# Performance work log

Hardware: AMD Instinct MI355X
Metric: run time of the kernel (lower is better)

The kernel has to match this reference:

```python
import jax, jax.numpy as jnp
import numpy as np
import math

B, S, D, H = 2, 2048, 1024, 16
HD = D // H            # head dim = 64
E, K = 8, 2            # routed experts, top-k
HM = 1024              # moe_inter_dim (multiple_of=256 keeps it)
HS = 1024              # shared expert hidden = moe_inter_dim * n_shared_experts
EPS = 1e-6
TEMP = 1.0


def setup_inputs() -> dict:
    key = jax.random.key(0)
    ks = jax.random.split(key, 16)
    s = 0.02
    x = jax.random.normal(ks[0], (B, S, D), jnp.float32)
    # RoPE angles: theta = 10000
    inv_freq = 1.0 / (10000.0 ** (np.arange(0, HD, 2, dtype=np.float32) / HD))  # (HD//2,)
    ang = np.arange(S, dtype=np.float32)[:, None] * inv_freq[None, :]           # (S, HD//2)
    freqs_cos = jnp.asarray(np.cos(ang))
    freqs_sin = jnp.asarray(np.sin(ang))
    return {
        "x": x,
        "freqs_cos": freqs_cos,
        "freqs_sin": freqs_sin,
        "att_norm_w": jnp.ones((D,), jnp.float32),
        "ffn_norm_w": jnp.ones((D,), jnp.float32),
        "wq": jax.random.normal(ks[1], (D, D), jnp.float32) * s,
        "wk": jax.random.normal(ks[2], (D, D), jnp.float32) * s,
        "wv": jax.random.normal(ks[3], (D, D), jnp.float32) * s,
        "wo": jax.random.normal(ks[4], (D, D), jnp.float32) * s,
        "gate_w": jax.random.normal(ks[5], (E, D), jnp.float32) * s,
        "ew1": jax.random.normal(ks[6], (E, D, HM), jnp.float32) * s,
        "ew2": jax.random.normal(ks[7], (E, HM, D), jnp.float32) * s,
        "ew3": jax.random.normal(ks[8], (E, D, HM), jnp.float32) * s,
        "sw1": jax.random.normal(ks[9], (D, HS), jnp.float32) * s,
        "sw2": jax.random.normal(ks[10], (HS, D), jnp.float32) * s,
        "sw3": jax.random.normal(ks[11], (D, HS), jnp.float32) * s,
    }


def _rmsnorm(x, w):
    return x * jax.lax.rsqrt(jnp.mean(x * x, axis=-1, keepdims=True) + EPS) * w


def _rope(t, cos, sin):
    # t: (B,H,S,HD); rotate pairs (even, odd) like complex multiply
    tr = t.reshape(B, H, S, HD // 2, 2)
    t0, t1 = tr[..., 0], tr[..., 1]
    c = cos[None, None, :, :]
    s_ = sin[None, None, :, :]
    o0 = t0 * c - t1 * s_
    o1 = t0 * s_ + t1 * c
    return jnp.stack([o0, o1], axis=-1).reshape(B, H, S, HD)


def reference(x, freqs_cos, freqs_sin, att_norm_w, ffn_norm_w,
              wq, wk, wv, wo, gate_w, ew1, ew2, ew3, sw1, sw2, sw3):
    # ---- attention sub-block ----
    xn = _rmsnorm(x, att_norm_w)
    q = (xn @ wq).reshape(B, S, H, HD).transpose(0, 2, 1, 3)  # (B,H,S,HD)
    k = (xn @ wk).reshape(B, S, H, HD).transpose(0, 2, 1, 3)
    v = (xn @ wv).reshape(B, S, H, HD).transpose(0, 2, 1, 3)
    q = _rope(q, freqs_cos, freqs_sin)
    k = _rope(k, freqs_cos, freqs_sin)
    scores = jnp.einsum('bhqd,bhkd->bhqk', q, k) / math.sqrt(HD)
    attn = jax.nn.softmax(scores, axis=-1)
    out = jnp.einsum('bhqk,bhkd->bhqd', attn, v)
    out = out.transpose(0, 2, 1, 3).reshape(B, S, D) @ wo
    h = x + out

    # ---- MoE sub-block ----
    xf = _rmsnorm(h, ffn_norm_w).reshape(-1, D)  # (N,D), N=B*S
    # shared expert (SwiGLU)
    shared = (jax.nn.silu(xf @ sw1) * (xf @ sw3)) @ sw2
    # gate (eval mode: no noise)
    g_scores = (xf @ gate_w.T) / TEMP
    probs = jax.nn.softmax(g_scores, axis=-1)          # (N,E)
    vals, idx = jax.lax.top_k(probs, K)                 # (N,K)
    vals = vals / (jnp.sum(vals, axis=-1, keepdims=True) + 1e-9)
    # per-token per-expert weight (equivalent to scatter into expert_mask)
    mask = jnp.sum(jax.nn.one_hot(idx, E, dtype=xf.dtype) * vals[..., None], axis=1)  # (N,E)
    # routed experts: dense per-expert SwiGLU, weighted combine (zero weight => no contribution)
    h1 = jax.nn.silu(jnp.einsum('nd,edh->enh', xf, ew1)) * jnp.einsum('nd,edh->enh', xf, ew3)
    eo = jnp.einsum('enh,ehd->end', h1, ew2)            # (E,N,D)
    y = jnp.einsum('end,ne->nd', eo, mask) + shared
    return h + y.reshape(B, S, D)
```

## Files before the change

### kernel.cpp

```cpp
#include <hip/hip_runtime.h>
#include <hip/hip_bf16.h>
#include <stdint.h>


typedef __hip_bfloat16 bf16;
typedef __attribute__((ext_vector_type(8))) __bf16 bf16x8;
typedef __attribute__((ext_vector_type(4))) float f32x4;
typedef __attribute__((ext_vector_type(2))) unsigned int u32x2;

#define S_  2048
#define D_  1024
#define N_  4096

__device__ __forceinline__ float b2f(bf16 h) { return __bfloat162float(h); }
__device__ __forceinline__ bf16  f2b(float f) { return __float2bfloat16(f); }

__device__ __forceinline__ bf16x8 ld_bf16x8(const bf16* p) {
    union { uint4 u; bf16x8 v; } x;
    x.u = *(const uint4*)p;
    return x.v;
}

__device__ __forceinline__ void gload_lds16(const void* gsrc, void* ldst) {
    __builtin_amdgcn_global_load_lds(
        (__attribute__((address_space(1))) void*)const_cast<void*>(gsrc),
        (__attribute__((address_space(3))) void*)ldst, 16, 0, 0);
}

__device__ __forceinline__ u32x2 tr16_read(unsigned lds_off) {
    u32x2 d;
    asm volatile("ds_read_b64_tr_b16 %0, %1" : "=v"(d) : "v"(lds_off));
    return d;
}

__global__ __launch_bounds__(256)
void transpose_all(const float* __restrict__ wq, const float* __restrict__ wk,
                   const float* __restrict__ wv, const float* __restrict__ wo,
                   const float* __restrict__ ew1, const float* __restrict__ ew2,
                   const float* __restrict__ ew3, const float* __restrict__ sw1,
                   const float* __restrict__ sw2, const float* __restrict__ sw3,
                   bf16* __restrict__ wqkv_t, bf16* __restrict__ wo_t,
                   bf16* __restrict__ ew13_t, bf16* __restrict__ ew2_t)
{
    __shared__ float t[32][33];
    const int z = blockIdx.z;
    const float* in; bf16* out; int rm = 1, ro = 0;
    if (z < 3)        { in = (z == 0 ? wq : z == 1 ? wk : wv); out = wqkv_t + (size_t)z * 1048576; }
    else if (z == 3)  { in = wo; out = wo_t; }
    else if (z < 12)  { const int e = z - 4;  in = ew1 + (size_t)e * 1048576; out = ew13_t + (size_t)e * 2097152; rm = 2; ro = 0; }
    else if (z < 20)  { const int e = z - 12; in = ew3 + (size_t)e * 1048576; out = ew13_t + (size_t)e * 2097152; rm = 2; ro = 1; }
    else if (z < 28)  { const int e = z - 20; in = ew2 + (size_t)e * 1048576; out = ew2_t + (size_t)e * 1048576; }
    else if (z == 28) { in = sw1; out = ew13_t + (size_t)8 * 2097152; rm = 2; ro = 0; }
    else if (z == 29) { in = sw3; out = ew13_t + (size_t)8 * 2097152; rm = 2; ro = 1; }
    else              { in = sw2; out = ew2_t + (size_t)8 * 1048576; }

    const int c0 = blockIdx.x * 32, r0 = blockIdx.y * 32;
    const int tx = threadIdx.x & 31, ty = threadIdx.x >> 5;
#pragma unroll
    for (int i = 0; i < 32; i += 8)
        t[ty + i][tx] = in[(size_t)(r0 + ty + i) * 1024 + c0 + tx];
    __syncthreads();
#pragma unroll
    for (int i = 0; i < 32; i += 8)
        out[(size_t)((c0 + ty + i) * rm + ro) * 1024 + r0 + tx] = f2b(t[tx][ty + i]);
}

__global__ __launch_bounds__(256)
void rmsnorm_kernel(const float* __restrict__ x, const float* __restrict__ w,
                    bf16* __restrict__ out)
{
    const int n = blockIdx.x;
    const int tid = threadIdx.x;
    const float4 v = *(const float4*)(x + (size_t)n * D_ + tid * 4);
    float ss = v.x * v.x + v.y * v.y + v.z * v.z + v.w * v.w;
#pragma unroll
    for (int m = 1; m < 64; m <<= 1) ss += __shfl_xor(ss, m);
    __shared__ float red[4];
    if ((tid & 63) == 0) red[tid >> 6] = ss;
    __syncthreads();
    const float tot = red[0] + red[1] + red[2] + red[3];
    const float rstd = rsqrtf(tot * (1.0f / D_) + 1e-6f);
    const float4 wv = *(const float4*)(w + tid * 4);
    union { bf16 h[4]; uint2 u; } pk;
    pk.h[0] = f2b(v.x * rstd * wv.x);
    pk.h[1] = f2b(v.y * rstd * wv.y);
    pk.h[2] = f2b(v.z * rstd * wv.z);
    pk.h[3] = f2b(v.w * rstd * wv.w);
    *(uint2*)(out + (size_t)n * D_ + tid * 4) = pk.u;
}

template<int EPI, int MODE>
__global__ __launch_bounds__(256)
void gemm_bt(const bf16* __restrict__ A, const bf16* __restrict__ Bt,
             void* __restrict__ Cout, const float* __restrict__ resid,
             int M, int Kdim, int lda, int ldb, int ldc, long bstride,
             const int* __restrict__ tlist, const int* __restrict__ offs,
             const float* __restrict__ fc, const float* __restrict__ fs)
{
    __shared__ bf16 As[128 * 32];
    __shared__ bf16 Bs[128 * 32];
    const int tid = threadIdx.x;
    const int wave = tid >> 6, lane = tid & 63;

    int bx, by;
    if constexpr (MODE == 0) {
        const int gx = gridDim.x;
        const int nwg = gx * gridDim.y;
        int flat = blockIdx.y * gx + blockIdx.x;
        flat = (flat & 7) * (nwg >> 3) + (flat >> 3);
        bx = flat % gx; by = flat / gx;
    } else {
        bx = blockIdx.x; by = blockIdx.y;
    }

    int mcount = M, outBase = 0;
    const bf16* Bp = Bt;
    if (MODE != 0) {
        const int e = blockIdx.z;
        outBase = offs[e];
        mcount = offs[e + 1] - outBase;
        Bp = Bt + (size_t)e * bstride;
    }
    const int m0 = by * 128;
    if (m0 >= mcount) return;
    const int n0 = bx * 128;

    const int srow = tid >> 2;
    const int scol = (tid & 3) * 8;
    const bf16* aptr[2];
    const bf16* bptr[2];
#pragma unroll
    for (int i = 0; i < 2; i++) {
        int r = m0 + i * 64 + srow;
        if (r >= mcount) r = mcount - 1;
        long arow;
        if (MODE == 1)      arow = tlist[outBase + r];
        else if (MODE == 2) arow = (long)outBase + r;
        else                arow = r;
        aptr[i] = A + (size_t)arow * lda + scol;
        bptr[i] = Bp + (size_t)(n0 + i * 64 + srow) * ldb + scol;
    }

    f32x4 zero4 = {0.f, 0.f, 0.f, 0.f};
    f32x4 acc[4][4];
#pragma unroll
    for (int m = 0; m < 4; m++)
#pragma unroll
        for (int n = 0; n < 4; n++) acc[m][n] = zero4;

    const int wm = (wave >> 1) * 64, wn = (wave & 1) * 64;
    const int fr = lane & 15, fk = (lane >> 4) * 8;
    const int aoff = (wm + fr) * 32 + fk;
    const int boff = (wn + fr) * 32 + fk;

    for (int kt = 0; kt < Kdim; kt += 32) {
        __syncthreads();
#pragma unroll
        for (int i = 0; i < 2; i++) {
            gload_lds16(aptr[i] + kt, (char*)As + i * 4096 + wave * 1024);
            gload_lds16(bptr[i] + kt, (char*)Bs + i * 4096 + wave * 1024);
        }
        __syncthreads();
        bf16x8 af[4], bfr[4];
#pragma unroll
        for (int m = 0; m < 4; m++) af[m] = ld_bf16x8(&As[aoff + m * 512]);
#pragma unroll
        for (int n = 0; n < 4; n++) bfr[n] = ld_bf16x8(&Bs[boff + n * 512]);
#pragma unroll
        for (int m = 0; m < 4; m++)
#pragma unroll
            for (int n = 0; n < 4; n++)
                acc[m][n] = __builtin_amdgcn_mfma_f32_16x16x32_bf16(af[m], bfr[n], acc[m][n], 0, 0, 0);
    }

    const int crow = m0 + wm + (lane >> 4) * 4;
    const int ccol = n0 + wn + fr;
#pragma unroll
    for (int m = 0; m < 4; m++)
#pragma unroll
        for (int n = 0; n < 4; n++)
#pragma unroll
            for (int j = 0; j < 4; j++) {
                const int r = crow + m * 16 + j;
                const int c = ccol + n * 16;
                const float v = acc[m][n][j];
                if (EPI == 3) {
                    const float other = __shfl_xor(v, 1);
                    const float res = (v / (1.f + __expf(-v))) * other;
                    if (((lane & 1) == 0) && r < mcount)
                        ((bf16*)Cout)[(size_t)(outBase + r) * ldc + (c >> 1)] = f2b(res);
                } else if (EPI == 4) {
                    const float other = __shfl_xor(v, 1);
                    float o = v;
                    if (c < 2048) {
                        const int s = r & (S_ - 1);
                        const int jf = (c & 63) >> 1;
                        const float co = fc[s * 32 + jf], si = fs[s * 32 + jf];
                        o = v * co + other * ((c & 1) ? si : -si);
                        if (c < 1024) o *= 0.125f;
                    }
                    ((bf16*)Cout)[(size_t)r * ldc + c] = f2b(o);
                } else if (r < mcount) {
                    const size_t oi = (size_t)(outBase + r) * ldc + c;
                    if (EPI == 0)      ((bf16*)Cout)[oi] = f2b(v);
                    else if (EPI == 1) ((float*)Cout)[oi] = v;
                    else               ((float*)Cout)[oi] = resid[oi] + v;
                }
            }
}

__global__ __launch_bounds__(256)
void attn_kernel(const bf16* __restrict__ qkv, bf16* __restrict__ out)
{
    __shared__ __align__(16) bf16 Ks[64 * 72];
    __shared__ __align__(16) bf16 Vs[4 * 1032 + 8];
    const int tid = threadIdx.x, wave = tid >> 6, lane = tid & 63;
    const int b = blockIdx.z, hh = blockIdx.y;
    const int q0 = blockIdx.x * 128;
    const bf16* base  = qkv + ((size_t)b * S_) * 3072 + (size_t)hh * 64;
    const bf16* kbase = base + 1024;
    const bf16* vbase = base + 2048;
    const int fr = lane & 15, fg = lane >> 4;

    bf16x8 aq[2][2];
#pragma unroll
    for (int qb = 0; qb < 2; qb++)
#pragma unroll
        for (int s2 = 0; s2 < 2; s2++)
            aq[qb][s2] = ld_bf16x8(base + (size_t)(q0 + wave * 32 + qb * 16 + fr) * 3072 + s2 * 32 + fg * 8);

    f32x4 zero4 = {0.f, 0.f, 0.f, 0.f};
    f32x4 acc_o[2][4];
    float mrow[2], lrow[2];
#pragma unroll
    for (int qb = 0; qb < 2; qb++) {
#pragma unroll
        for (int hf = 0; hf < 4; hf++) acc_o[qb][hf] = zero4;
        mrow[qb] = -1e30f; lrow[qb] = 0.f;
    }

    const int srow = tid >> 2, sc4 = tid & 3;
    const unsigned vtr0 =
        (unsigned)(uintptr_t)(__attribute__((address_space(3))) void*)&Vs[0] + lane * 8;

    uint4 kg0, kg1, vg0, vg1;
    {
        const bf16* kr = kbase + (size_t)srow * 3072 + sc4 * 16;
        kg0 = *(const uint4*)kr; kg1 = *(const uint4*)(kr + 8);
        const bf16* vr = vbase + (size_t)srow * 3072 + sc4 * 16;
        vg0 = *(const uint4*)vr; vg1 = *(const uint4*)(vr + 8);
    }

    for (int kv0 = 0; kv0 < S_; kv0 += 64) {
        __syncthreads();
        *(uint4*)&Ks[srow * 72 + sc4 * 16]         = kg0;
        *(uint4*)&Ks[srow * 72 + sc4 * 16 + 8]     = kg1;
        *(uint4*)&Vs[sc4 * 1032 + srow * 16]       = vg0;
        *(uint4*)&Vs[sc4 * 1032 + srow * 16 + 8]   = vg1;
        __syncthreads();
        if (kv0 + 64 < S_) {
            const bf16* kr = kbase + (size_t)(kv0 + 64 + srow) * 3072 + sc4 * 16;
            kg0 = *(const uint4*)kr; kg1 = *(const uint4*)(kr + 8);
            const bf16* vr = vbase + (size_t)(kv0 + 64 + srow) * 3072 + sc4 * 16;
            vg0 = *(const uint4*)vr; vg1 = *(const uint4*)(vr + 8);
        }

        f32x4 sc[4][2];
#pragma unroll
        for (int kt = 0; kt < 4; kt++)
#pragma unroll
            for (int qb = 0; qb < 2; qb++) sc[kt][qb] = zero4;
        __builtin_amdgcn_s_setprio(1);
#pragma unroll
        for (int kt = 0; kt < 4; kt++) {
            const bf16x8 k0 = ld_bf16x8(&Ks[(kt * 16 + fr) * 72 + fg * 8]);
            const bf16x8 k1 = ld_bf16x8(&Ks[(kt * 16 + fr) * 72 + 32 + fg * 8]);
#pragma unroll
            for (int qb = 0; qb < 2; qb++) {
                sc[kt][qb] = __builtin_amdgcn_mfma_f32_16x16x32_bf16(k0, aq[qb][0], sc[kt][qb], 0, 0, 0);
                sc[kt][qb] = __builtin_amdgcn_mfma_f32_16x16x32_bf16(k1, aq[qb][1], sc[kt][qb], 0, 0, 0);
            }
        }
        __builtin_amdgcn_s_setprio(0);

        bf16x8 pcomb[2][2];
        float scalv[2];
#pragma unroll
        for (int qb = 0; qb < 2; qb++) {
            float pm = -1e30f;
#pragma unroll
            for (int kt = 0; kt < 4; kt++)
#pragma unroll
                for (int j = 0; j < 4; j++) pm = fmaxf(pm, sc[kt][qb][j]);
            pm = fmaxf(pm, __shfl_xor(pm, 16));
            pm = fmaxf(pm, __shfl_xor(pm, 32));
            const float mnew = fmaxf(mrow[qb], pm);
            const float scal = __expf(mrow[qb] - mnew);
            mrow[qb] = mnew;
            float ps = 0.f;
            union { bf16 h[16]; bf16x8 v8[2]; } pk;
#pragma unroll
            for (int kt = 0; kt < 4; kt++)
#pragma unroll
                for (int j = 0; j < 4; j++) {
                    const float p = __expf(sc[kt][qb][j] - mnew);
                    ps += p;
                    pk.h[kt * 4 + j] = f2b(p);
                }
            pcomb[qb][0] = pk.v8[0];
            pcomb[qb][1] = pk.v8[1];
            ps += __shfl_xor(ps, 16);
            ps += __shfl_xor(ps, 32);
            lrow[qb] = lrow[qb] * scal + ps;
            scalv[qb] = scal;
        }

#pragma unroll
        for (int j = 0; j < 4; j++) {
            const int src = (lane & 48) + fg * 4 + j;
            const float s0 = __shfl(scalv[0], src);
            const float s1 = __shfl(scalv[1], src);
#pragma unroll
            for (int hf = 0; hf < 4; hf++) {
                acc_o[0][hf][j] *= s0;
                acc_o[1][hf][j] *= s1;
            }
        }

#pragma unroll
        for (int tp = 0; tp < 2; tp++) {
            union { u32x2 d2[2]; bf16x8 v8; } vc[4];
#pragma unroll
            for (int hf = 0; hf < 4; hf++) {
                vc[hf].d2[0] = tr16_read(vtr0 + hf * 2064 + (tp * 2)     * 512);
                vc[hf].d2[1] = tr16_read(vtr0 + hf * 2064 + (tp * 2 + 1) * 512);
            }
            asm volatile("s_waitcnt lgkmcnt(0)" ::: "memory");
            __builtin_amdgcn_sched_barrier(0);
            __builtin_amdgcn_s_setprio(1);
#pragma unroll
            for (int hf = 0; hf < 4; hf++)
#pragma unroll
                for (int qb = 0; qb < 2; qb++)
                    acc_o[qb][hf] = __builtin_amdgcn_mfma_f32_16x16x32_bf16(
                        pcomb[qb][tp], vc[hf].v8, acc_o[qb][hf], 0, 0, 0);
            __builtin_amdgcn_s_setprio(0);
        }
    }

#pragma unroll
    for (int qb = 0; qb < 2; qb++) {
        const float inv = 1.f / lrow[qb];
#pragma unroll
        for (int j = 0; j < 4; j++) {
            const float ij = __shfl(inv, (lane & 48) + fg * 4 + j);
            const int r = q0 + wave * 32 + qb * 16 + fg * 4 + j;
#pragma unroll
            for (int hf = 0; hf < 4; hf++)
                out[((size_t)(b * S_ + r)) * D_ + hh * 64 + hf * 16 + fr] =
                    f2b(acc_o[qb][hf][j] * ij);
        }
    }
}

__global__ __launch_bounds__(256)
void gating_kernel(const float* __restrict__ h, const float* __restrict__ gw,
                   const float* __restrict__ wnorm,
                   int* __restrict__ top_idx, float* __restrict__ top_w)
{
    const int wave = threadIdx.x >> 6, lane = threadIdx.x & 63;
    const int n = blockIdx.x * 4 + wave;
    const float* hr = h + (size_t)n * D_;
    float acc[8] = {0.f, 0.f, 0.f, 0.f, 0.f, 0.f, 0.f, 0.f};
    float ss = 0.f;
    for (int d = lane * 4; d < D_; d += 256) {
        const float4 hv = *(const float4*)(hr + d);
        const float4 wv = *(const float4*)(wnorm + d);
        ss += hv.x * hv.x + hv.y * hv.y + hv.z * hv.z + hv.w * hv.w;
        const float x0 = hv.x * wv.x, x1 = hv.y * wv.y, x2 = hv.z * wv.z, x3 = hv.w * wv.w;
#pragma unroll
        for (int e2 = 0; e2 < 8; e2++) {
            const float4 gv = *(const float4*)(gw + e2 * D_ + d);
            acc[e2] += x0 * gv.x + x1 * gv.y + x2 * gv.z + x3 * gv.w;
        }
    }
#pragma unroll
    for (int m = 1; m < 64; m <<= 1) {
        ss += __shfl_xor(ss, m);
#pragma unroll
        for (int e2 = 0; e2 < 8; e2++) acc[e2] += __shfl_xor(acc[e2], m);
    }
    if (lane == 0) {
        const float rstd = rsqrtf(ss * (1.0f / D_) + 1e-6f);
        float s[8];
#pragma unroll
        for (int e2 = 0; e2 < 8; e2++) s[e2] = acc[e2] * rstd;
        int e0 = 0;
#pragma unroll
        for (int e2 = 1; e2 < 8; e2++) if (s[e2] > s[e0]) e0 = e2;
        int e1 = (e0 == 0) ? 1 : 0;
#pragma unroll
        for (int e2 = 0; e2 < 8; e2++) if (e2 != e0 && s[e2] > s[e1]) e1 = e2;
        const float mx = s[e0];
        float Z = 0.f;
        float p[8];
#pragma unroll
        for (int e2 = 0; e2 < 8; e2++) { p[e2] = __expf(s[e2] - mx); Z += p[e2]; }
        const float v0 = p[e0] / Z, v1 = p[e1] / Z;
        const float sm = v0 + v1 + 1e-9f;
        top_idx[n * 2] = e0; top_idx[n * 2 + 1] = e1;
        top_w[n * 2] = v0 / sm; top_w[n * 2 + 1] = v1 / sm;
    }
}

__global__ __launch_bounds__(1024)
void route_kernel(const int* __restrict__ top_idx, int* __restrict__ offs,
                  int* __restrict__ token_list, int* __restrict__ tok_pos)
{
    __shared__ int hist[8];
    __shared__ int base[8];
    const int tid = threadIdx.x;
    if (tid < 8) hist[tid] = 0;
    __syncthreads();
    int4 e4a = *(const int4*)(top_idx + tid * 8);
    int4 e4b = *(const int4*)(top_idx + tid * 8 + 4);
    int myidx[8] = {e4a.x, e4a.y, e4a.z, e4a.w, e4b.x, e4b.y, e4b.z, e4b.w};
#pragma unroll
    for (int i = 0; i < 8; i++) atomicAdd(&hist[myidx[i]], 1);
    __syncthreads();
    if (tid == 0) {
        int o = 0;
#pragma unroll
        for (int e = 0; e < 8; e++) { base[e] = o; offs[e] = o; o += hist[e]; }
        offs[8] = o;
        offs[9] = o + N_;
    }
    __syncthreads();
    if (tid < 8) hist[tid] = 0;
    __syncthreads();
#pragma unroll
    for (int i = 0; i < 8; i++) {
        const int entry = tid * 8 + i;
        const int e = myidx[i];
        const int pos = base[e] + atomicAdd(&hist[e], 1);
        token_list[pos] = entry >> 1;
        tok_pos[entry] = pos;
    }
#pragma unroll
    for (int i = 0; i < 4; i++)
        token_list[2 * N_ + tid * 4 + i] = tid * 4 + i;
}

__global__ __launch_bounds__(256)
void combine_kernel(const float* __restrict__ h, const bf16* __restrict__ eo,
                    const int* __restrict__ tok_pos, const float* __restrict__ top_w,
                    float* __restrict__ out)
{
    const int idx = blockIdx.x * 256 + threadIdx.x;
    const int n = idx >> 8;
    const int c = (idx & 255) * 4;
    const float4 hv = *(const float4*)(h + (size_t)n * D_ + c);
    const int p0 = tok_pos[n * 2], p1 = tok_pos[n * 2 + 1];
    const float w0 = top_w[n * 2], w1 = top_w[n * 2 + 1];
    union { uint2 u; bf16 hh[4]; } a0, a1, ash;
    a0.u  = *(const uint2*)(eo + (size_t)p0 * D_ + c);
    a1.u  = *(const uint2*)(eo + (size_t)p1 * D_ + c);
    ash.u = *(const uint2*)(eo + (size_t)(2 * N_ + n) * D_ + c);
    float4 r;
    r.x = hv.x + b2f(ash.hh[0]) + w0 * b2f(a0.hh[0]) + w1 * b2f(a1.hh[0]);
    r.y = hv.y + b2f(ash.hh[1]) + w0 * b2f(a0.hh[1]) + w1 * b2f(a1.hh[1]);
    r.z = hv.z + b2f(ash.hh[2]) + w0 * b2f(a0.hh[2]) + w1 * b2f(a1.hh[2]);
    r.w = hv.w + b2f(ash.hh[3]) + w0 * b2f(a0.hh[3]) + w1 * b2f(a1.hh[3]);
    *(float4*)(out + (size_t)n * D_ + c) = r;
}

extern "C" void kernel_launch(void* const* d_in, const int* in_sizes, int n_in,
                              void* d_out, int out_size, void* d_ws, size_t ws_size,
                              hipStream_t stream)
{
    const float* x   = (const float*)d_in[0];
    const float* fc  = (const float*)d_in[1];
    const float* fs  = (const float*)d_in[2];
    const float* anw = (const float*)d_in[3];
    const float* fnw = (const float*)d_in[4];
    const float* wq  = (const float*)d_in[5];
    const float* wk  = (const float*)d_in[6];
    const float* wv  = (const float*)d_in[7];
    const float* wo  = (const float*)d_in[8];
    const float* gw  = (const float*)d_in[9];
    const float* ew1 = (const float*)d_in[10];
    const float* ew2 = (const float*)d_in[11];
    const float* ew3 = (const float*)d_in[12];
    const float* sw1 = (const float*)d_in[13];
    const float* sw2 = (const float*)d_in[14];
    const float* sw3 = (const float*)d_in[15];

    char* ws = (char*)d_ws;
    bf16*  wqkv_t = (bf16*)(ws + 0);
    bf16*  wo_t   = (bf16*)(ws + 6291456);
    bf16*  ew13_t = (bf16*)(ws + 8388608);
    bf16*  ew2_t  = (bf16*)(ws + 46137344);
    bf16*  xn     = (bf16*)(ws + 65011712);
    bf16*  qkv    = (bf16*)(ws + 73400320);
    bf16*  attn   = (bf16*)(ws + 98566144);
    float* hbuf   = (float*)(ws + 106954752);
    bf16*  eo     = (bf16*)(ws + 123731968);
    char*  misc   = ws + 148897792;
    int*   offs       = (int*)(misc + 0);
    int*   top_idx    = (int*)(misc + 128);
    float* top_w      = (float*)(misc + 128 + 32768);
    int*   token_list = (int*)(misc + 128 + 65536);
    int*   tok_pos    = (int*)(misc + 128 + 131072);

    const dim3 tb(256);
    transpose_all<<<dim3(32, 32, 31), tb, 0, stream>>>(
        wq, wk, wv, wo, ew1, ew2, ew3, sw1, sw2, sw3,
        wqkv_t, wo_t, ew13_t, ew2_t);

    rmsnorm_kernel<<<N_, tb, 0, stream>>>(x, anw, xn);
    gemm_bt<4, 0><<<dim3(24, 32, 1), tb, 0, stream>>>(xn, wqkv_t, qkv, nullptr,
        N_, 1024, 1024, 1024, 3072, 0, nullptr, nullptr, fc, fs);
    attn_kernel<<<dim3(16, 16, 2), tb, 0, stream>>>(qkv, attn);
    gemm_bt<2, 0><<<dim3(8, 32, 1), tb, 0, stream>>>(attn, wo_t, hbuf, x,
        N_, 1024, 1024, 1024, 1024, 0, nullptr, nullptr, nullptr, nullptr);

    rmsnorm_kernel<<<N_, tb, 0, stream>>>(hbuf, fnw, xn);
    gating_kernel<<<N_ / 4, tb, 0, stream>>>(hbuf, gw, fnw, top_idx, top_w);
    route_kernel<<<1, 1024, 0, stream>>>(top_idx, offs, token_list, tok_pos);

    gemm_bt<3, 1><<<dim3(16, 32, 9), tb, 0, stream>>>(xn, ew13_t, qkv, nullptr,
        0, 1024, 1024, 1024, 1024, 2097152, token_list, offs, nullptr, nullptr);
    gemm_bt<0, 2><<<dim3(8, 32, 9), tb, 0, stream>>>((const bf16*)qkv, ew2_t, eo, nullptr,
        0, 1024, 1024, 1024, 1024, 1048576, nullptr, offs, nullptr, nullptr);

    combine_kernel<<<4096, tb, 0, stream>>>(hbuf, eo, tok_pos, top_w, (float*)d_out);
}
```

Measured before the change: 408.3 us.

## Double-buffer LDS tiles in GEMM to overlap global loads with MFMA

Splits the shared-memory A/B tiles into two buffers and issues the global-to-LDS loads for the next K slice before computing on the current one. Partial waitcnt (vmcnt(4)) plus raw s_barrier replace the two __syncthreads per iteration, so load latency can hide behind MFMA work. LDS use doubles to 32KB per block, which may lower occupancy. The hand-written waitcnt/barrier sequence depends on compiler instruction ordering; if the compiler does not emit exactly the expected loads, it risks subtle races.

```diff
diff --git a/kernel.cpp b/kernel.cpp
--- a/kernel.cpp
+++ b/kernel.cpp
@@ -97,8 +97,8 @@
              const int* __restrict__ tlist, const int* __restrict__ offs,
              const float* __restrict__ fc, const float* __restrict__ fs)
 {
-    __shared__ bf16 As[128 * 32];
-    __shared__ bf16 Bs[128 * 32];
+    __shared__ bf16 As[2][128 * 32];
+    __shared__ bf16 Bs[2][128 * 32];
     const int tid = threadIdx.x;
     const int wave = tid >> 6, lane = tid & 63;
 
@@ -153,24 +153,43 @@
     const int aoff = (wm + fr) * 32 + fk;
     const int boff = (wn + fr) * 32 + fk;
 
-    for (int kt = 0; kt < Kdim; kt += 32) {
-        __syncthreads();
-#pragma unroll
-        for (int i = 0; i < 2; i++) {
-            gload_lds16(aptr[i] + kt, (char*)As + i * 4096 + wave * 1024);
-            gload_lds16(bptr[i] + kt, (char*)Bs + i * 4096 + wave * 1024);
-        }
-        __syncthreads();
+    const int nkt = Kdim >> 5;
+#pragma unroll
+    for (int i = 0; i < 2; i++) {
+        gload_lds16(aptr[i], (char*)&As[0][0] + i * 4096 + wave * 1024);
+        gload_lds16(bptr[i], (char*)&Bs[0][0] + i * 4096 + wave * 1024);
+    }
+
+    int p = 0;
+    for (int kt = 0; kt < nkt; kt++) {
+        if (kt + 1 < nkt) {
+            const int ko = (kt + 1) << 5;
+#pragma unroll
+            for (int i = 0; i < 2; i++) {
+                gload_lds16(aptr[i] + ko, (char*)&As[p ^ 1][0] + i * 4096 + wave * 1024);
+                gload_lds16(bptr[i] + ko, (char*)&Bs[p ^ 1][0] + i * 4096 + wave * 1024);
+            }
+            asm volatile("s_waitcnt vmcnt(4)" ::: "memory");
+        } else {
+            asm volatile("s_waitcnt vmcnt(0)" ::: "memory");
+        }
+        asm volatile("s_barrier" ::: "memory");
+
+        const bf16* Ab = &As[p][0];
+        const bf16* Bb = &Bs[p][0];
         bf16x8 af[4], bfr[4];
 #pragma unroll
-        for (int m = 0; m < 4; m++) af[m] = ld_bf16x8(&As[aoff + m * 512]);
-#pragma unroll
-        for (int n = 0; n < 4; n++) bfr[n] = ld_bf16x8(&Bs[boff + n * 512]);
+        for (int m = 0; m < 4; m++) af[m] = ld_bf16x8(&Ab[aoff + m * 512]);
+#pragma unroll
+        for (int n = 0; n < 4; n++) bfr[n] = ld_bf16x8(&Bb[boff + n * 512]);
 #pragma unroll
         for (int m = 0; m < 4; m++)
 #pragma unroll
             for (int n = 0; n < 4; n++)
                 acc[m][n] = __builtin_amdgcn_mfma_f32_16x16x32_bf16(af[m], bfr[n], acc[m][n], 0, 0, 0);
+
+        asm volatile("s_barrier" ::: "memory");
+        p ^= 1;
     }
 
     const int crow = m0 + wm + (lane >> 4) * 4;
```

Measured after the change: 391.8 us. 1.04x faster.
